# Kernel optimization log

Measured on AMD Instinct MI355X. Metric: run time of the kernel, lower is better.

## Reference

```python
import jax, jax.numpy as jnp
import numpy as np

HEAD_DIM = 64
NUM_HEADS = 32
ROPE_THETA = 10000.0


def _rope_cos_sin(seq_len, dim, theta, dtype):
    inv_freq = 1.0 / (theta ** (jnp.arange(0, dim, 2, dtype=jnp.float32) / dim))
    t = jnp.arange(seq_len, dtype=jnp.float32)
    freqs = jnp.outer(t, inv_freq)  # [T, dim/2]
    return jnp.cos(freqs).astype(dtype), jnp.sin(freqs).astype(dtype)


def _apply_rope(x, cos, sin):
    # x: [B, T, H, D]; GPT-NeoX style (split halves), matching flash-attn rotary (interleaved=False)
    d2 = x.shape[-1] // 2
    x1, x2 = x[..., :d2], x[..., d2:]
    c = cos[None, :, None, :]
    s = sin[None, :, None, :]
    return jnp.concatenate([x1 * c - x2 * s, x2 * c + x1 * s], axis=-1)


def setup_inputs() -> dict:
    key = jax.random.key(0)
    ks = jax.random.split(key, 8)
    B, T, Dm = 2, 2048, 2048
    H, Dh = NUM_HEADS, HEAD_DIM
    sc = 1.0 / np.sqrt(Dm)
    return {
        "hidden_states": jax.random.normal(ks[0], (B, T, Dm), jnp.float32),
        "v1": jax.random.normal(ks[1], (B, T, H, Dh), jnp.float32),
        "lambda1": jax.random.uniform(ks[2], (), jnp.float32),
        "Wq": jax.random.normal(ks[3], (Dm, Dm), jnp.float32) * sc,
        "Wk": jax.random.normal(ks[4], (Dm, Dm), jnp.float32) * sc,
        "Wv": jax.random.normal(ks[5], (Dm, Dm), jnp.float32) * sc,
        "Wo": jax.random.normal(ks[6], (Dm, Dm), jnp.float32) * sc,
        "lambda2": jnp.float32(0.5),
    }


def reference(hidden_states, v1, lambda1, Wq, Wk, Wv, Wo, lambda2):
    B, T, Dm = hidden_states.shape
    H, Dh = NUM_HEADS, HEAD_DIM
    # QKV projections + head split
    q = (hidden_states @ Wq).reshape(B, T, H, Dh)
    k = (hidden_states @ Wk).reshape(B, T, H, Dh)
    v = (hidden_states @ Wv).reshape(B, T, H, Dh)
    # Value residual mixing: V' = lambda1 * V_1 + lambda2 * V_n
    v = lambda1 * v1 + lambda2 * v
    # RoPE (seqlen_offset = 0, no cache)
    cos, sin = _rope_cos_sin(T, Dh, ROPE_THETA, q.dtype)
    q = _apply_rope(q, cos, sin)
    k = _apply_rope(k, cos, sin)
    # Causal attention (flash_attn_func(..., causal=True) equivalent)
    scale = 1.0 / np.sqrt(Dh)
    scores = jnp.einsum("bqhd,bkhd->bhqk", q, k) * scale
    causal = jnp.tril(jnp.ones((T, T), dtype=bool))
    scores = jnp.where(causal[None, None], scores, jnp.finfo(scores.dtype).min)
    probs = jax.nn.softmax(scores, axis=-1)
    o = jnp.einsum("bhqk,bkhd->bqhd", probs, v).reshape(B, T, Dm)
    return o @ Wo
```

## Files before the change

### kernel.cpp

```cpp
#include <hip/hip_runtime.h>
#include <hip/hip_bf16.h>
#include <math.h>

typedef __bf16 bf16;
typedef __bf16 bf16x8 __attribute__((ext_vector_type(8)));
typedef __bf16 bf16x4 __attribute__((ext_vector_type(4)));
typedef float  f32x4  __attribute__((ext_vector_type(4)));
typedef short  sv4    __attribute__((ext_vector_type(4)));

#define B_  2
#define T_  2048
#define DM  2048
#define H_  32
#define DH  64

__device__ __forceinline__ bf16x8 load8(const bf16* p) {
    return *reinterpret_cast<const bf16x8*>(p);
}

__device__ __forceinline__ void gld16(const bf16* g, bf16* l) {
    __builtin_amdgcn_global_load_lds(
        (const __attribute__((address_space(1))) unsigned int*)g,
        (__attribute__((address_space(3))) unsigned int*)l, 16, 0, 0);
}

__global__ void k_convert(const float* __restrict__ in, bf16* __restrict__ out, int n4) {
    int i = blockIdx.x * blockDim.x + threadIdx.x;
    if (i < n4) {
        float4 v = reinterpret_cast<const float4*>(in)[i];
        bf16x4 o;
        o[0] = (bf16)v.x; o[1] = (bf16)v.y; o[2] = (bf16)v.z; o[3] = (bf16)v.w;
        reinterpret_cast<bf16x4*>(out)[i] = o;
    }
}

__global__ void k_transposeW(const float* __restrict__ Wq, const float* __restrict__ Wk,
                             const float* __restrict__ Wv, const float* __restrict__ Wo,
                             bf16* __restrict__ WqT, bf16* __restrict__ WkT,
                             bf16* __restrict__ WvT, bf16* __restrict__ WoT) {
    const float* in; bf16* out;
    switch (blockIdx.z) {
        case 0: in = Wq; out = WqT; break;
        case 1: in = Wk; out = WkT; break;
        case 2: in = Wv; out = WvT; break;
        default: in = Wo; out = WoT; break;
    }
    __shared__ float tile[32][33];
    int tx = threadIdx.x, ty = threadIdx.y;
    int x0 = blockIdx.x * 32, y0 = blockIdx.y * 32;
    #pragma unroll
    for (int i = 0; i < 4; i++)
        tile[ty + i*8][tx] = in[(size_t)(y0 + ty + i*8) * DM + x0 + tx];
    __syncthreads();
    #pragma unroll
    for (int i = 0; i < 4; i++)
        out[(size_t)(x0 + ty + i*8) * DM + y0 + tx] = (bf16)tile[tx][ty + i*8];
}

template<int OUT_BF16>
__global__ __launch_bounds__(256)
void k_gemm(const bf16* __restrict__ A, const bf16* __restrict__ BT,
            void* __restrict__ Cout, int ldc) {
    constexpr int K = 2048;
    __shared__ bf16 ldsA[128 * 32];
    __shared__ bf16 ldsB[128 * 32];
    int tid = threadIdx.x;
    int lane = tid & 63, w = tid >> 6;
    int l16 = lane & 15, quad = lane >> 4;
    int wm = w >> 1, wn = w & 1;
    int mblk = blockIdx.y * 128, nblk = blockIdx.x * 128;

    f32x4 acc[4][4] = {};

    int sgz = ((lane & 3) ^ ((lane >> 3) & 3)) * 8;
    const bf16* gA = A  + (size_t)(mblk + w * 32 + (lane >> 2)) * K + sgz;
    const bf16* gB = BT + (size_t)(nblk + w * 32 + (lane >> 2)) * K + sgz;
    bf16* lA = ldsA + w * 1024;
    bf16* lB = ldsB + w * 1024;
    int sA = (quad ^ ((l16 >> 1) & 3)) * 8;

    for (int k0 = 0; k0 < K; k0 += 32) {
        gld16(gA + k0,          lA);
        gld16(gA + 16 * K + k0, lA + 512);
        gld16(gB + k0,          lB);
        gld16(gB + 16 * K + k0, lB + 512);
        __syncthreads();
        bf16x8 af[4], bfr[4];
        #pragma unroll
        for (int s = 0; s < 4; s++)
            af[s] = *reinterpret_cast<bf16x8*>(&ldsA[(wm * 64 + s * 16 + l16) * 32 + sA]);
        #pragma unroll
        for (int t = 0; t < 4; t++)
            bfr[t] = *reinterpret_cast<bf16x8*>(&ldsB[(wn * 64 + t * 16 + l16) * 32 + sA]);
        #pragma unroll
        for (int s = 0; s < 4; s++)
            #pragma unroll
            for (int t = 0; t < 4; t++)
                acc[s][t] = __builtin_amdgcn_mfma_f32_16x16x32_bf16(af[s], bfr[t], acc[s][t], 0, 0, 0);
        __syncthreads();
    }

    #pragma unroll
    for (int s = 0; s < 4; s++) {
        int row = mblk + wm * 64 + s * 16 + quad * 4;
        #pragma unroll
        for (int t = 0; t < 4; t++) {
            int col = nblk + wn * 64 + t * 16 + l16;
            #pragma unroll
            for (int r = 0; r < 4; r++) {
                if (OUT_BF16)
                    reinterpret_cast<bf16*>(Cout)[(size_t)(row + r) * ldc + col] = (bf16)acc[s][t][r];
                else
                    reinterpret_cast<float*>(Cout)[(size_t)(row + r) * ldc + col] = acc[s][t][r];
            }
        }
    }
}

__global__ void k_tab(float2* __restrict__ tab) {
    int id = blockIdx.x * 256 + threadIdx.x;
    int i = id & 31, t = id >> 5;
    float inv = __builtin_amdgcn_exp2f(-(float)i * 0.41524101186092037f);
    float ang = (float)t * inv;
    float s, c;
    __sincosf(ang, &s, &c);
    tab[id] = make_float2(c, s);
}

__global__ void k_rope(bf16* __restrict__ qkv, const float2* __restrict__ tab) {
    int id = blockIdx.x * 256 + threadIdx.x;
    int j   = id & 3;
    int h   = (id >> 2) & 31;
    int sel = (id >> 7) & 1;
    int t   = (id >> 8) & 2047;
    int b   = id >> 19;
    size_t base = ((size_t)(b * T_ + t)) * 6144 + sel * 2048 + h * 64 + j * 8;
    bf16x8 x1 = load8(qkv + base);
    bf16x8 x2 = load8(qkv + base + 32);
    const float2* tp = tab + t * 32 + j * 8;
    bf16x8 o1, o2;
    #pragma unroll
    for (int e = 0; e < 8; e++) {
        float c = tp[e].x, s = tp[e].y;
        float a = (float)x1[e], v = (float)x2[e];
        o1[e] = (bf16)(a * c - v * s);
        o2[e] = (bf16)(v * c + a * s);
    }
    *reinterpret_cast<bf16x8*>(qkv + base)      = o1;
    *reinterpret_cast<bf16x8*>(qkv + base + 32) = o2;
}

__global__ void k_combinev(const float* __restrict__ v1, const bf16* __restrict__ qkv,
                           const float* __restrict__ l1p, const float* __restrict__ l2p,
                           bf16* __restrict__ vT) {
    __shared__ float tile[64 * 33];
    float l1 = l1p[0], l2 = l2p[0];
    int b = blockIdx.y >> 5, h = blockIdx.y & 31;
    int t0 = blockIdx.x * 32;
    int tid = threadIdx.x;
    int d = tid & 63, tr = tid >> 6;
    #pragma unroll
    for (int i = 0; i < 8; i++) {
        int t = t0 + i * 4 + tr;
        size_t iv1 = ((size_t)(b * T_ + t)) * 2048 + h * 64 + d;
        size_t ivg = ((size_t)(b * T_ + t)) * 6144 + 4096 + h * 64 + d;
        tile[d * 33 + i * 4 + tr] = l1 * v1[iv1] + l2 * (float)qkv[ivg];
    }
    __syncthreads();
    int tl = tid & 31, dr = tid >> 5;
    #pragma unroll
    for (int j = 0; j < 8; j++) {
        int d2 = dr + j * 8;
        vT[((size_t)((b * H_ + h) * 64 + d2)) * T_ + t0 + tl] = (bf16)tile[d2 * 33 + tl];
    }
}

__global__ __launch_bounds__(256)
void k_attn(const bf16* __restrict__ qkv, const bf16* __restrict__ vT, bf16* __restrict__ o) {
    __shared__ bf16 ldsK[64 * 64];
    __shared__ bf16 ldsV[64 * 64];
    int bx = blockIdx.x;
    int bh = blockIdx.y;
    int b = bh >> 5, h = bh & 31;
    int tid = threadIdx.x;
    int lane = tid & 63, w = tid >> 6;
    int l16 = lane & 15, quad = lane >> 4;

    int rl = lane >> 3, sg = ((lane & 7) ^ rl) * 8;
    const bf16* kgl = qkv + ((size_t)(b * T_) + w * 16 + rl) * 6144 + 2048 + h * 64 + sg;
    const bf16* vgl = vT + ((size_t)bh * DH + w * 16 + rl) * T_ + sg;
    bf16* lKw = ldsK + w * 16 * 64;
    bf16* lVw = ldsV + w * 16 * 64;

    int skey = (quad ^ (l16 & 7)) * 8;
    int skey2 = ((quad + 4) ^ (l16 & 7)) * 8;

    #pragma unroll 1
    for (int pass = 0; pass < 2; pass++) {
        int qt = pass ? (31 - bx) : bx;
        int qbase = qt * 64 + w * 16;

        size_t qrow = (size_t)(b * T_ + qbase + l16) * 6144 + h * 64;
        bf16x8 qf[2];
        #pragma unroll
        for (int half = 0; half < 2; half++) {
            bf16x8 v = load8(qkv + qrow + half * 32 + quad * 8);
            #pragma unroll
            for (int e = 0; e < 8; e++) v[e] = (bf16)((float)v[e] * 0.1803368801f);
            qf[half] = v;
        }

        f32x4 accO[4] = {};
        float m_ = -1e30f, pl = 0.f;

        int nkt = qt + 1;
        for (int kt = 0; kt < nkt; kt++) {
            int key0 = kt * 64;
            #pragma unroll
            for (int j = 0; j < 2; j++) {
                gld16(kgl + (size_t)(key0 + j * 8) * 6144, lKw + j * 512);
                gld16(vgl + (size_t)(j * 8) * T_ + key0,   lVw + j * 512);
            }
            __syncthreads();

            bool diag = (kt == qt);
            f32x4 st[4];
            sv4 pk[4];
            #pragma unroll
            for (int ks = 0; ks < 4; ks++) {
                if (!diag || key0 + ks * 16 <= qbase + 15) {
                    bf16x8 kf0 = *reinterpret_cast<bf16x8*>(&ldsK[(ks * 16 + l16) * 64 + skey]);
                    bf16x8 kf1 = *reinterpret_cast<bf16x8*>(&ldsK[(ks * 16 + l16) * 64 + skey2]);
                    f32x4 z = {};
                    z = __builtin_amdgcn_mfma_f32_16x16x32_bf16(kf0, qf[0], z, 0, 0, 0);
                    z = __builtin_amdgcn_mfma_f32_16x16x32_bf16(kf1, qf[1], z, 0, 0, 0);
                    st[ks] = z;
                } else {
                    st[ks] = (f32x4){-3e38f, -3e38f, -3e38f, -3e38f};
                }
            }

            if (diag) {
                int qcol = qbase + l16;
                #pragma unroll
                for (int ks = 0; ks < 4; ks++)
                    #pragma unroll
                    for (int r = 0; r < 4; r++)
                        if (key0 + ks * 16 + quad * 4 + r > qcol) st[ks][r] = -3e38f;
            }

            float mx = st[0][0];
            #pragma unroll
            for (int ks = 0; ks < 4; ks++)
                #pragma unroll
                for (int r = 0; r < 4; r++) mx = fmaxf(mx, st[ks][r]);
            mx = fmaxf(mx, __shfl_xor(mx, 16));
            mx = fmaxf(mx, __shfl_xor(mx, 32));
            if (__any(mx > m_)) {
                float nm = fmaxf(m_, mx);
                float alpha = __builtin_amdgcn_exp2f(m_ - nm);
                m_ = nm;
                pl *= alpha;
                #pragma unroll
                for (int n2 = 0; n2 < 4; n2++) accO[n2] *= alpha;
            }
            float rsum = 0.f;
            #pragma unroll
            for (int ks = 0; ks < 4; ks++) {
                bf16x4 ph;
                #pragma unroll
                for (int r = 0; r < 4; r++) {
                    float p = __builtin_amdgcn_exp2f(st[ks][r] - m_);
                    rsum += p;
                    ph[r] = (bf16)p;
                }
                pk[ks] = __builtin_bit_cast(sv4, ph);
            }
            pl += rsum;

            #pragma unroll
            for (int ks = 0; ks < 4; ks++) {
                if (!diag || key0 + ks * 16 <= qbase + 15) {
                    int svf = ((ks * 2 + (quad >> 1)) ^ (l16 & 7)) * 8 + (quad & 1) * 4;
                    #pragma unroll
                    for (int n2 = 0; n2 < 4; n2++) {
                        sv4 vf = *reinterpret_cast<sv4*>(&ldsV[(n2 * 16 + l16) * 64 + svf]);
                        accO[n2] = __builtin_amdgcn_mfma_f32_16x16x16bf16_1k(
                            vf, pk[ks], accO[n2], 0, 0, 0);
                    }
                }
            }
            __syncthreads();
        }

        float l = pl;
        l += __shfl_xor(l, 16);
        l += __shfl_xor(l, 32);
        float inv = 1.0f / l;
        int query = qbase + l16;
        #pragma unroll
        for (int n2 = 0; n2 < 4; n2++) {
            bf16x4 ov;
            #pragma unroll
            for (int r = 0; r < 4; r++) ov[r] = (bf16)(accO[n2][r] * inv);
            *reinterpret_cast<bf16x4*>(
                &o[(size_t)(b * T_ + query) * DM + h * 64 + n2 * 16 + quad * 4]) = ov;
        }
    }
}

extern "C" void kernel_launch(void* const* d_in, const int* in_sizes, int n_in,
                              void* d_out, int out_size, void* d_ws, size_t ws_size,
                              hipStream_t stream) {
    const float* hs   = (const float*)d_in[0];
    const float* v1   = (const float*)d_in[1];
    const float* lam1 = (const float*)d_in[2];
    const float* Wq   = (const float*)d_in[3];
    const float* Wk   = (const float*)d_in[4];
    const float* Wv   = (const float*)d_in[5];
    const float* Wo   = (const float*)d_in[6];
    const float* lam2 = (const float*)d_in[7];

    char* ws = (char*)d_ws;
    bf16* hs_bf = (bf16*)(ws);
    float2* tab = (float2*)(ws);
    bf16* Wcat  = (bf16*)(ws + 16777216);
    bf16* WoT   = (bf16*)(ws + 41943040);
    bf16* qkv   = (bf16*)(ws + 50331648);
    bf16* vT_bf = (bf16*)(ws + 100663296);
    bf16* o_bf  = (bf16*)(ws + 117440512);

    k_convert<<<8192, 256, 0, stream>>>(hs, hs_bf, 2097152);
    k_transposeW<<<dim3(64, 64, 4), dim3(32, 8), 0, stream>>>(
        Wq, Wk, Wv, Wo, Wcat, Wcat + 4194304, Wcat + 8388608, WoT);

    k_gemm<1><<<dim3(48, 32), 256, 0, stream>>>(hs_bf, Wcat, (void*)qkv, 6144);

    k_tab<<<256, 256, 0, stream>>>(tab);
    k_rope<<<4096, 256, 0, stream>>>(qkv, tab);

    k_combinev<<<dim3(64, 64), 256, 0, stream>>>(v1, qkv, lam1, lam2, vT_bf);

    k_attn<<<dim3(16, 64), 256, 0, stream>>>(qkv, vT_bf, o_bf);

    k_gemm<0><<<dim3(16, 32), 256, 0, stream>>>(o_bf, WoT, d_out, 2048);
}
```

Before: 445.8 us.

## Add 256x256-tile ping-pong GEMM with 8 waves for QKV projection

Adds a new bf16 GEMM kernel with 256x256 output tiles, 512 threads and double-buffered LDS filled by direct global-to-LDS loads with an XOR swizzle. It uses barrier-interleaved MFMA phases with s_setprio, and explicit vmcnt waits overlap the next tile's loads with compute. The QKV projection now launches this kernel instead of the 128x128 one, cutting global traffic per FLOP. The risks are fewer blocks (384) on a 256-CU device, which can leave CUs unevenly loaded, and high register pressure from 32 accumulators per thread.

New measurement: 442.0 us. No clear change (-0.9%).

```diff
diff --git a/kernel.cpp b/kernel.cpp
--- a/kernel.cpp
+++ b/kernel.cpp
@@ -117,6 +117,108 @@
     }
 }
 
+template<int OUT_BF16>
+__global__ __launch_bounds__(512, 2)
+void k_gemm256(const bf16* __restrict__ A, const bf16* __restrict__ BT,
+               void* __restrict__ Cout, int ldc) {
+    constexpr int K = 2048;
+    __shared__ bf16 lds[32768];
+    const int tid  = threadIdx.x;
+    const int lane = tid & 63, w = tid >> 6;
+    const int l16  = lane & 15, quad = lane >> 4;
+    const int wm   = w >> 2, wn = w & 3;
+    const size_t mblk = (size_t)blockIdx.y * 256, nblk = (size_t)blockIdx.x * 256;
+
+    f32x4 acc[8][4] = {};
+
+    const int sg = (((tid & 3) ^ ((tid >> 3) & 3)) << 3);
+    const bf16* gA = A  + (mblk + (tid >> 2)) * K + sg;
+    const bf16* gB = BT + (nblk + (tid >> 2)) * K + sg;
+
+    const int segr = ((quad ^ ((l16 >> 1) & 3)) << 3);
+    const int aoff = (wm * 128 + l16) * 32 + segr;
+    const int boff = (wn * 64  + l16) * 32 + segr;
+
+#define STGA(kt_) do { \
+    const bf16* g_ = gA + (kt_) * 32; \
+    bf16* l_ = lds + ((((kt_) & 1) << 14) + 8192) + w * 512; \
+    gld16(g_, l_); gld16(g_ + 128 * 2048, l_ + 4096); \
+} while (0)
+
+#define STGB(kt_) do { \
+    const bf16* g_ = gB + (kt_) * 32; \
+    bf16* l_ = lds + (((kt_) & 1) << 14) + w * 512; \
+    gld16(g_, l_); gld16(g_ + 128 * 2048, l_ + 4096); \
+} while (0)
+
+#define LD4(dst_, base_) do { \
+    _Pragma("unroll") for (int i_ = 0; i_ < 4; ++i_) \
+        dst_[i_] = *reinterpret_cast<const bf16x8*>((base_) + i_ * 512); \
+} while (0)
+
+#define MFMA16(mh_) do { \
+    _Pragma("unroll") for (int mi_ = 0; mi_ < 4; ++mi_) \
+        _Pragma("unroll") for (int ni_ = 0; ni_ < 4; ++ni_) \
+            acc[(mh_) * 4 + mi_][ni_] = __builtin_amdgcn_mfma_f32_16x16x32_bf16( \
+                af[mi_], bq[ni_], acc[(mh_) * 4 + mi_][ni_], 0, 0, 0); \
+} while (0)
+
+#define BAR  __builtin_amdgcn_s_barrier()
+#define PRI1 __builtin_amdgcn_s_setprio(1)
+#define PRI0 __builtin_amdgcn_s_setprio(0)
+#define VM2  asm volatile("s_waitcnt vmcnt(2)" ::: "memory")
+#define VM0  asm volatile("s_waitcnt vmcnt(0)" ::: "memory")
+
+#define TILE(cb_, S0_, S1_, VM_) do { \
+    const bf16* rb_ = lds + (cb_) + boff; \
+    const bf16* ra_ = lds + (cb_) + 8192 + aoff; \
+    bf16x8 af[4], bq[4]; \
+    LD4(af, ra_); LD4(bq, rb_); \
+    S0_; BAR; PRI1; MFMA16(0); PRI0; BAR; \
+    LD4(af, ra_ + 2048); \
+    S1_; BAR; PRI1; MFMA16(1); PRI0; VM_; BAR; \
+} while (0)
+
+    STGB(0); STGA(0); STGB(1);
+    VM2;
+    BAR;
+
+    #pragma unroll 1
+    for (int t = 0; t < 61; t += 2) {
+        TILE(0,     STGA(t + 1), STGB(t + 2), VM2);
+        TILE(16384, STGA(t + 2), STGB(t + 3), VM2);
+    }
+    TILE(0,     STGA(63), (void)0, VM0);
+    TILE(16384, (void)0, (void)0, (void)0);
+
+#undef STGA
+#undef STGB
+#undef LD4
+#undef MFMA16
+#undef BAR
+#undef PRI1
+#undef PRI0
+#undef VM2
+#undef VM0
+#undef TILE
+
+    #pragma unroll
+    for (int mt = 0; mt < 8; ++mt) {
+        size_t row = mblk + wm * 128 + mt * 16 + quad * 4;
+        #pragma unroll
+        for (int nt = 0; nt < 4; ++nt) {
+            size_t col = nblk + wn * 64 + nt * 16 + l16;
+            #pragma unroll
+            for (int r = 0; r < 4; ++r) {
+                if (OUT_BF16)
+                    reinterpret_cast<bf16*>(Cout)[(row + r) * (size_t)ldc + col] = (bf16)acc[mt][nt][r];
+                else
+                    reinterpret_cast<float*>(Cout)[(row + r) * (size_t)ldc + col] = acc[mt][nt][r];
+            }
+        }
+    }
+}
+
 __global__ void k_tab(float2* __restrict__ tab) {
     int id = blockIdx.x * 256 + threadIdx.x;
     int i = id & 31, t = id >> 5;
@@ -334,7 +436,7 @@
     k_transposeW<<<dim3(64, 64, 4), dim3(32, 8), 0, stream>>>(
         Wq, Wk, Wv, Wo, Wcat, Wcat + 4194304, Wcat + 8388608, WoT);
 
-    k_gemm<1><<<dim3(48, 32), 256, 0, stream>>>(hs_bf, Wcat, (void*)qkv, 6144);
+    k_gemm256<1><<<dim3(24, 16), 512, 0, stream>>>(hs_bf, Wcat, (void*)qkv, 6144);
 
     k_tab<<<256, 256, 0, stream>>>(tab);
     k_rope<<<4096, 256, 0, stream>>>(qkv, tab);
```
